# Kernel optimization log

Hardware: AMD Instinct MI355X
Metric: run time of the kernel (lower is better)

Reference implementation:

```python
import jax, jax.numpy as jnp
import numpy as np

N_NODES = 50000
N_EDGES = 1600000
N_PAIRS = 4096
IN_N, IN_E = 32, 8
H, OE, ON = 4, 8, 32  # heads, out_edge_feats, out_node_feats
L = 4  # layers


def setup_inputs() -> dict:
    key = jax.random.key(0)
    ks = jax.random.split(key, 20)
    s = 0.1
    return {
        "x": jax.random.normal(ks[0], (N_NODES, IN_N), jnp.float32),
        "e": jax.random.normal(ks[1], (N_EDGES, IN_E), jnp.float32),
        "W_ni": jax.random.normal(ks[2], (L, IN_N, H * OE), jnp.float32) * s,
        "W_nj": jax.random.normal(ks[3], (L, IN_N, H * OE), jnp.float32) * s,
        "W_fij": jax.random.normal(ks[4], (L, IN_E, H * OE), jnp.float32) * s,
        "b_edge": jax.random.normal(ks[5], (L, H * OE), jnp.float32) * s,
        "attn": jax.random.normal(ks[6], (L, H, OE), jnp.float32) * s,
        "W_node": jax.random.normal(ks[7], (L, IN_N, H * ON), jnp.float32) * s,
        "W1": jax.random.normal(ks[8], (2 * L * ON, 128), jnp.float32) * s,
        "b1": jax.random.normal(ks[9], (128,), jnp.float32) * s,
        "W2": jax.random.normal(ks[10], (128, 1), jnp.float32) * s,
        "b2": jax.random.normal(ks[11], (1,), jnp.float32) * s,
        "src": jax.random.randint(ks[12], (N_EDGES,), 0, N_NODES, jnp.int32),
        "dst": jax.random.randint(ks[13], (N_EDGES,), 0, N_NODES, jnp.int32),
        "users": jax.random.randint(ks[14], (N_PAIRS,), 0, N_NODES, jnp.int32),
        "items": jax.random.randint(ks[15], (N_PAIRS,), 0, N_NODES, jnp.int32),
    }


def _egat_layer(h, e, src, dst, W_ni, W_nj, W_fij, b_edge, attn, W_node, n_nodes):
    # per-edge edge features: f_ni[src] + f_nj[dst] + f_fij + bias  -> (E, H*OE)
    f = (h @ W_ni)[src] + (h @ W_nj)[dst] + e @ W_fij + b_edge
    f_out = jax.nn.leaky_relu(f).reshape(-1, H, OE)          # (E, H, OE)
    logits = jnp.einsum("ehd,hd->eh", f_out, attn)           # (E, H)
    # edge softmax over incoming edges of each dst node
    mx = jax.ops.segment_max(logits, dst, num_segments=n_nodes)
    z = jnp.exp(logits - mx[dst])
    denom = jax.ops.segment_sum(z, dst, num_segments=n_nodes)
    a = z / denom[dst]                                        # (E, H)
    hh = (h @ W_node).reshape(n_nodes, H, ON)                 # (N, H, ON)
    msg = hh[src] * a[:, :, None]                             # (E, H, ON)
    return jax.ops.segment_sum(msg, dst, num_segments=n_nodes)  # (N, H, ON)


def reference(x, e, W_ni, W_nj, W_fij, b_edge, attn, W_node, W1, b1, W2, b2,
              src, dst, users, items):
    n_nodes = x.shape[0]
    states = []
    h = x
    for l in range(L):
        agg = _egat_layer(h, e, src, dst, W_ni[l], W_nj[l], W_fij[l],
                          b_edge[l], attn[l], W_node[l], n_nodes)
        h = jax.nn.elu(agg.sum(axis=1))  # sum heads, ELU -> (N, ON)
        states.append(h)
    states = jnp.concatenate(states, axis=1)                  # (N, L*ON)
    z = jnp.concatenate([states[users], states[items]], axis=1)  # (B, 2*L*ON)
    z = jax.nn.relu(z @ W1 + b1)
    out = jax.nn.sigmoid(z @ W2 + b2)
    return out[:, 0]
```

## Files before the change

### kernel.cpp

```cpp
#include <hip/hip_runtime.h>
#include <math.h>


static __device__ inline unsigned short f2bf(float f) {
  unsigned x = __float_as_uint(f);
  unsigned r = x + 0x7fffu + ((x >> 16) & 1u);
  return (unsigned short)(r >> 16);
}
static __device__ inline unsigned pack2bf(float lo, float hi) {
  return (unsigned)f2bf(lo) | ((unsigned)f2bf(hi) << 16);
}
static __device__ inline float bf_lo(unsigned u) {
  return __uint_as_float(u << 16);
}
static __device__ inline float bf_hi(unsigned u) {
  return __uint_as_float(u & 0xffff0000u);
}


__global__ void zero_ints(int* __restrict__ p, int n) {
  int i = blockIdx.x * blockDim.x + threadIdx.x;
  if (i < n) p[i] = 0;
}

__global__ void histogram(const int* __restrict__ dst, int* __restrict__ hist,
                          int n_edges) {
  int e = blockIdx.x * blockDim.x + threadIdx.x;
  if (e < n_edges) atomicAdd(&hist[dst[e]], 1);
}

__global__ void scan_block(const int* __restrict__ hist, int* __restrict__ partial,
                           int* __restrict__ blocksum, int n) {
  __shared__ int buf[1024];
  int tid = threadIdx.x;
  int g = blockIdx.x * 1024 + tid;
  int v = (g < n) ? hist[g] : 0;
  buf[tid] = v;
  __syncthreads();
  for (int off = 1; off < 1024; off <<= 1) {
    int t = (tid >= off) ? buf[tid - off] : 0;
    __syncthreads();
    buf[tid] += t;
    __syncthreads();
  }
  if (g < n) partial[g] = buf[tid] - v;
  if (tid == 1023) blocksum[blockIdx.x] = buf[1023];
}

__global__ void scan_sums(int* __restrict__ blocksum, int nb) {
  if (threadIdx.x == 0 && blockIdx.x == 0) {
    int run = 0;
    for (int i = 0; i < nb; i++) {
      int t = blocksum[i];
      blocksum[i] = run;
      run += t;
    }
    blocksum[nb] = run;
  }
}

__global__ void scan_add(int* __restrict__ partial ,
                         const int* __restrict__ blocksum,
                         int* __restrict__ cursor, int n, int nb) {
  int g = blockIdx.x * blockDim.x + threadIdx.x;
  if (g < n) {
    int val = partial[g] + blocksum[g >> 10];
    partial[g] = val;
    cursor[g] = val;
  }
  if (g == 0) partial[n] = blocksum[nb];
}

#define FILL_NR 8
__global__ void fill_perm(const int* __restrict__ dst, int* __restrict__ cursor,
                          int* __restrict__ perm, int n_edges, int seg) {
  int range = blockIdx.x % FILL_NR;
  int group = blockIdx.x / FILL_NR;
  int ngroups = gridDim.x / FILL_NR;
  int lo = range * seg;
  int hi = lo + seg;
  int stride = ngroups * blockDim.x;
  for (int k = group * blockDim.x + threadIdx.x; k < n_edges; k += stride) {
    int d = dst[k];
    if (d >= lo && d < hi) {
      int p = atomicAdd(&cursor[d], 1);
      perm[p] = k;
    }
  }
}

__global__ void expand_sorted(const int* __restrict__ perm,
                              const int* __restrict__ src,
                              const int* __restrict__ dst,
                              const float* __restrict__ e,
                              int* __restrict__ src_s, int* __restrict__ dst_s,
                              uint4* __restrict__ e_s, int n_edges) {
  int k = blockIdx.x * blockDim.x + threadIdx.x;
  if (k >= n_edges) return;
  int eid = perm[k];
  src_s[k] = src[eid];
  dst_s[k] = dst[eid];
  const float4* ep = (const float4*)(e + (size_t)eid * 8);
  float4 a = ep[0], b = ep[1];
  uint4 r;
  r.x = pack2bf(a.x, a.y); r.y = pack2bf(a.z, a.w);
  r.z = pack2bf(b.x, b.y); r.w = pack2bf(b.z, b.w);
  e_s[k] = r;
}


__global__ void node_proj(const float* __restrict__ h,
                          const float* __restrict__ Wni,
                          const float* __restrict__ Wnj,
                          const float* __restrict__ Wnode,
                          const float* __restrict__ bE,
                          unsigned short* __restrict__ fni,
                          unsigned short* __restrict__ cdst,
                          unsigned short* __restrict__ hh, int n_nodes) {
  int wave = (blockIdx.x * blockDim.x + threadIdx.x) >> 6;
  int lane = threadIdx.x & 63;
  int nwaves = (gridDim.x * blockDim.x) >> 6;
  int j = lane & 31;
  const float* Wsel = (lane < 32) ? Wni : Wnj;
  for (int n = wave; n < n_nodes; n += nwaves) {
    const float* hrow = h + (size_t)n * 32;
    float a0 = 0.f, a1 = 0.f, a2 = 0.f;
#pragma unroll
    for (int k = 0; k < 32; k++) {
      float hv = hrow[k];
      a0 += hv * Wsel[k * 32 + j];
      a1 += hv * Wnode[k * 128 + lane];
      a2 += hv * Wnode[k * 128 + lane + 64];
    }
    if (lane < 32) fni[(size_t)n * 32 + j] = f2bf(a0);
    else           cdst[(size_t)n * 32 + j] = f2bf(a0 + bE[j]);
    hh[(size_t)n * 128 + lane] = f2bf(a1);
    hh[(size_t)n * 128 + lane + 64] = f2bf(a2);
  }
}

__global__ void edge_z(const int* __restrict__ src_s,
                       const int* __restrict__ dst_s,
                       const uint4* __restrict__ e_s,
                       const unsigned short* __restrict__ fni,
                       const unsigned short* __restrict__ cdst,
                       const float* __restrict__ Wf,
                       const float* __restrict__ attn,
                       float4* __restrict__ zrec, int n_edges) {
  __shared__ float wfl[256];
  __shared__ float atl[32];
  int tid = threadIdx.x;
  wfl[tid] = Wf[tid];
  if (tid < 32) atl[tid] = attn[tid];
  __syncthreads();
  int k = blockIdx.x * blockDim.x + tid;
  if (k >= n_edges) return;
  int s = src_s[k], d = dst_s[k];
  uint4 ep = e_s[k];
  float ev[8];
  ev[0] = bf_lo(ep.x); ev[1] = bf_hi(ep.x);
  ev[2] = bf_lo(ep.y); ev[3] = bf_hi(ep.y);
  ev[4] = bf_lo(ep.z); ev[5] = bf_hi(ep.z);
  ev[6] = bf_lo(ep.w); ev[7] = bf_hi(ep.w);
  const uint4* fr = (const uint4*)(fni + (size_t)s * 32);
  const uint4* cr = (const uint4*)(cdst + (size_t)d * 32);
  float f[32];
#pragma unroll
  for (int q = 0; q < 4; q++) {
    uint4 ua = fr[q], ub = cr[q];
    const unsigned* uap = (const unsigned*)&ua;
    const unsigned* ubp = (const unsigned*)&ub;
#pragma unroll
    for (int c = 0; c < 4; c++) {
      int jj = q * 8 + c * 2;
      f[jj]     = bf_lo(uap[c]) + bf_lo(ubp[c]);
      f[jj + 1] = bf_hi(uap[c]) + bf_hi(ubp[c]);
    }
  }
#pragma unroll
  for (int kk = 0; kk < 8; kk++) {
    float ek = ev[kk];
#pragma unroll
    for (int j4 = 0; j4 < 8; j4++) {
      float4 w = ((const float4*)wfl)[kk * 8 + j4];
      f[j4 * 4 + 0] = fmaf(ek, w.x, f[j4 * 4 + 0]);
      f[j4 * 4 + 1] = fmaf(ek, w.y, f[j4 * 4 + 1]);
      f[j4 * 4 + 2] = fmaf(ek, w.z, f[j4 * 4 + 2]);
      f[j4 * 4 + 3] = fmaf(ek, w.w, f[j4 * 4 + 3]);
    }
  }
  float lg[4] = {0.f, 0.f, 0.f, 0.f};
#pragma unroll
  for (int jj = 0; jj < 32; jj++) {
    float t = f[jj];
    t = (t >= 0.f) ? t : 0.01f * t;
    lg[jj >> 3] = fmaf(t, atl[jj], lg[jj >> 3]);
  }
  zrec[k] = make_float4(__expf(lg[0]), __expf(lg[1]),
                        __expf(lg[2]), __expf(lg[3]));
}

__global__ void node_agg(const float4* __restrict__ zrec,
                         const int* __restrict__ src_s,
                         const int* __restrict__ row_off,
                         const unsigned* __restrict__ hh,
                         float* __restrict__ hcur,
                         float* __restrict__ states,
                         int l, int n_nodes) {
  __shared__ float zw[4][64 * 4];
  __shared__ int sw[4][64];
  int wid = threadIdx.x >> 6;
  int lane = threadIdx.x & 63;
  int n = (blockIdx.x * blockDim.x + threadIdx.x) >> 6;
  if (n >= n_nodes) return;
  int base = row_off[n], end = row_off[n + 1];
  int head = lane >> 4;
  float* zwf = zw[wid];
  int* swp = sw[wid];
  float accx = 0.f, accy = 0.f;
  float sz0 = 0.f, sz1 = 0.f, sz2 = 0.f, sz3 = 0.f;

  for (int chunk = base; chunk < end; chunk += 64) {
    int k = chunk + lane;
    float4 zv4 = make_float4(0.f, 0.f, 0.f, 0.f);
    int sv = 0;
    if (k < end) { zv4 = zrec[k]; sv = src_s[k]; }
    ((float4*)zwf)[lane] = zv4;
    swp[lane] = sv;
    sz0 += zv4.x; sz1 += zv4.y; sz2 += zv4.z; sz3 += zv4.w;
    int cnt = min(64, end - chunk);

    int ee = 0;
    for (; ee + 8 <= cnt; ee += 8) {
      unsigned u[8];
      float zl[8];
#pragma unroll
      for (int i = 0; i < 8; i++) {
        int ss = __builtin_amdgcn_readfirstlane(swp[ee + i]);
        zl[i] = zwf[(ee + i) * 4 + head];
        u[i] = hh[(size_t)ss * 64 + lane];
      }
#pragma unroll
      for (int i = 0; i < 8; i++) {
        accx = fmaf(bf_lo(u[i]), zl[i], accx);
        accy = fmaf(bf_hi(u[i]), zl[i], accy);
      }
    }
    for (; ee < cnt; ee++) {
      int ss = __builtin_amdgcn_readfirstlane(swp[ee]);
      float zv = zwf[ee * 4 + head];
      unsigned u = hh[(size_t)ss * 64 + lane];
      accx = fmaf(bf_lo(u), zv, accx);
      accy = fmaf(bf_hi(u), zv, accy);
    }
  }

#pragma unroll
  for (int off = 32; off > 0; off >>= 1) {
    sz0 += __shfl_xor(sz0, off); sz1 += __shfl_xor(sz1, off);
    sz2 += __shfl_xor(sz2, off); sz3 += __shfl_xor(sz3, off);
  }
  float dh = (head == 0) ? sz0 : (head == 1) ? sz1 : (head == 2) ? sz2 : sz3;

  float vx = 0.f, vy = 0.f;
  if (dh > 0.f) { vx = accx / dh; vy = accy / dh; }
  vx += __shfl_xor(vx, 16); vx += __shfl_xor(vx, 32);
  vy += __shfl_xor(vy, 16); vy += __shfl_xor(vy, 32);
  if (lane < 16) {
    float rx = (vx > 0.f) ? vx : expm1f(vx);
    float ry = (vy > 0.f) ? vy : expm1f(vy);
    float2 r = make_float2(rx, ry);
    ((float2*)(hcur + (size_t)n * 32))[lane] = r;
    ((float2*)(states + (size_t)n * 128 + l * 32))[lane] = r;
  }
}

__global__ void mlp_head(const float* __restrict__ states,
                         const int* __restrict__ users, const int* __restrict__ items,
                         const float* __restrict__ W1, const float* __restrict__ b1,
                         const float* __restrict__ W2, const float* __restrict__ b2,
                         float* __restrict__ out, int n_pairs) {
  __shared__ float zin[256];
  __shared__ float red[2];
  int p = blockIdx.x;
  if (p >= n_pairs) return;
  int t = threadIdx.x;
  int u = users[p], it = items[p];
  zin[t] = states[(size_t)u * 128 + t];
  zin[t + 128] = states[(size_t)it * 128 + t];
  __syncthreads();
  float acc = b1[t];
#pragma unroll 8
  for (int i = 0; i < 256; i++) acc += zin[i] * W1[i * 128 + t];
  acc = acc > 0.f ? acc : 0.f;
  float c = acc * W2[t];
#pragma unroll
  for (int off = 32; off > 0; off >>= 1) c += __shfl_down(c, off);
  if ((t & 63) == 0) red[t >> 6] = c;
  __syncthreads();
  if (t == 0) {
    float sum = red[0] + red[1] + b2[0];
    out[p] = 1.f / (1.f + expf(-sum));
  }
}


extern "C" void kernel_launch(void* const* d_in, const int* in_sizes, int n_in,
                              void* d_out, int out_size, void* d_ws, size_t ws_size,
                              hipStream_t stream) {
  const float* x     = (const float*)d_in[0];
  const float* e     = (const float*)d_in[1];
  const float* W_ni  = (const float*)d_in[2];
  const float* W_nj  = (const float*)d_in[3];
  const float* W_fij = (const float*)d_in[4];
  const float* b_e   = (const float*)d_in[5];
  const float* attn  = (const float*)d_in[6];
  const float* W_nd  = (const float*)d_in[7];
  const float* W1    = (const float*)d_in[8];
  const float* b1    = (const float*)d_in[9];
  const float* W2    = (const float*)d_in[10];
  const float* b2    = (const float*)d_in[11];
  const int* src   = (const int*)d_in[12];
  const int* dst   = (const int*)d_in[13];
  const int* users = (const int*)d_in[14];
  const int* items = (const int*)d_in[15];
  float* out = (float*)d_out;

  int n_nodes = in_sizes[0] / 32;
  int n_edges = in_sizes[12];
  int n_pairs = in_sizes[14];

  char* wsb = (char*)d_ws;
  size_t off = 0;
  auto alloc = [&](size_t bytes) {
    char* p = wsb + off;
    off = (off + bytes + 255) & ~(size_t)255;
    return p;
  };
  float*          hcur   = (float*)alloc((size_t)n_nodes * 32 * 4);
  float*          states = (float*)alloc((size_t)n_nodes * 128 * 4);
  unsigned short* fni    = (unsigned short*)alloc((size_t)n_nodes * 32 * 2);
  unsigned short* cdst   = (unsigned short*)alloc((size_t)n_nodes * 32 * 2);
  unsigned short* hh     = (unsigned short*)alloc((size_t)n_nodes * 128 * 2);
  uint4*          e_s    = (uint4*)alloc((size_t)n_edges * 16);
  float4*         zrec   = (float4*)alloc((size_t)n_edges * 16);
  int*            src_s  = (int*)alloc((size_t)n_edges * 4);
  int*            dst_s  = (int*)alloc((size_t)n_edges * 4);
  int*            row_off  = (int*)alloc(((size_t)n_nodes + 8) * 4);
  int*            blocksum = (int*)alloc(256 * 4);
  int* perm   = (int*)zrec;
  int* hist   = (int*)((char*)zrec + ((size_t)n_edges * 4 + 1024));
  int* cursor = (int*)((char*)zrec + ((size_t)n_edges * 8 + 2048));

  int nb = (n_nodes + 1023) / 1024;
  int seg = (n_nodes + FILL_NR - 1) / FILL_NR;
  zero_ints<<<(n_nodes + 255) / 256, 256, 0, stream>>>(hist, n_nodes);
  histogram<<<(n_edges + 255) / 256, 256, 0, stream>>>(dst, hist, n_edges);
  scan_block<<<nb, 1024, 0, stream>>>(hist, row_off, blocksum, n_nodes);
  scan_sums<<<1, 64, 0, stream>>>(blocksum, nb);
  scan_add<<<(n_nodes + 255) / 256, 256, 0, stream>>>(row_off, blocksum, cursor,
                                                      n_nodes, nb);
  fill_perm<<<2048, 256, 0, stream>>>(dst, cursor, perm, n_edges, seg);
  expand_sorted<<<(n_edges + 255) / 256, 256, 0, stream>>>(
      perm, src, dst, e, src_s, dst_s, e_s, n_edges);

  for (int l = 0; l < 4; l++) {
    const float* hin = (l == 0) ? x : hcur;
    node_proj<<<2048, 256, 0, stream>>>(hin, W_ni + l * 1024, W_nj + l * 1024,
                                        W_nd + l * 4096, b_e + l * 32,
                                        fni, cdst, hh, n_nodes);
    edge_z<<<(n_edges + 255) / 256, 256, 0, stream>>>(
        src_s, dst_s, e_s, fni, cdst, W_fij + l * 256, attn + l * 32,
        zrec, n_edges);
    node_agg<<<(n_nodes * 64 + 255) / 256, 256, 0, stream>>>(
        zrec, src_s, row_off, (const unsigned*)hh, hcur, states, l, n_nodes);
  }
  mlp_head<<<n_pairs, 128, 0, stream>>>(states, users, items, W1, b1, W2, b2,
                                        out, n_pairs);
}
```

Baseline: 904.5 us.

## Split aggregation per head with head-planar layouts and XCD-aware block mapping

Stores hh and edge z values in head-major planes and replaces the single all-heads aggregation with a per-head kernel. Block indices are mapped so each XCD handles one head, which shrinks the gather working set per L2. A separate combine kernel sums the heads and applies ELU, states are stored as bf16, and the src/dst permutation is folded into fill_perm. The cost is an extra kernel launch per layer, an extra bf16 round trip for per-head partial results, and reduced precision.

```diff
diff --git a/kernel.cpp b/kernel.cpp
--- a/kernel.cpp
+++ b/kernel.cpp
@@ -9,6 +9,9 @@
 }
 static __device__ inline unsigned pack2bf(float lo, float hi) {
   return (unsigned)f2bf(lo) | ((unsigned)f2bf(hi) << 16);
+}
+static __device__ inline float bf2f(unsigned short u) {
+  return __uint_as_float(((unsigned)u) << 16);
 }
 static __device__ inline float bf_lo(unsigned u) {
   return __uint_as_float(u << 16);
@@ -72,8 +75,10 @@
 }
 
 #define FILL_NR 8
-__global__ void fill_perm(const int* __restrict__ dst, int* __restrict__ cursor,
-                          int* __restrict__ perm, int n_edges, int seg) {
+__global__ void fill_perm3(const int* __restrict__ dst, const int* __restrict__ src,
+                           int* __restrict__ cursor, int* __restrict__ perm,
+                           int* __restrict__ src_s, int* __restrict__ dst_s,
+                           int n_edges, int seg) {
   int range = blockIdx.x % FILL_NR;
   int group = blockIdx.x / FILL_NR;
   int ngroups = gridDim.x / FILL_NR;
@@ -85,21 +90,17 @@
     if (d >= lo && d < hi) {
       int p = atomicAdd(&cursor[d], 1);
       perm[p] = k;
-    }
-  }
-}
-
-__global__ void expand_sorted(const int* __restrict__ perm,
-                              const int* __restrict__ src,
-                              const int* __restrict__ dst,
-                              const float* __restrict__ e,
-                              int* __restrict__ src_s, int* __restrict__ dst_s,
-                              uint4* __restrict__ e_s, int n_edges) {
+      src_s[p] = src[k];
+      dst_s[p] = d;
+    }
+  }
+}
+
+__global__ void expand_e(const int* __restrict__ perm, const float* __restrict__ e,
+                         uint4* __restrict__ e_s, int n_edges) {
   int k = blockIdx.x * blockDim.x + threadIdx.x;
   if (k >= n_edges) return;
   int eid = perm[k];
-  src_s[k] = src[eid];
-  dst_s[k] = dst[eid];
   const float4* ep = (const float4*)(e + (size_t)eid * 8);
   float4 a = ep[0], b = ep[1];
   uint4 r;
@@ -116,11 +117,12 @@
                           const float* __restrict__ bE,
                           unsigned short* __restrict__ fni,
                           unsigned short* __restrict__ cdst,
-                          unsigned short* __restrict__ hh, int n_nodes) {
+                          unsigned short* __restrict__ hh_t, int n_nodes) {
   int wave = (blockIdx.x * blockDim.x + threadIdx.x) >> 6;
   int lane = threadIdx.x & 63;
   int nwaves = (gridDim.x * blockDim.x) >> 6;
   int j = lane & 31;
+  size_t plane = (size_t)n_nodes * 32;
   const float* Wsel = (lane < 32) ? Wni : Wnj;
   for (int n = wave; n < n_nodes; n += nwaves) {
     const float* hrow = h + (size_t)n * 32;
@@ -134,8 +136,10 @@
     }
     if (lane < 32) fni[(size_t)n * 32 + j] = f2bf(a0);
     else           cdst[(size_t)n * 32 + j] = f2bf(a0 + bE[j]);
-    hh[(size_t)n * 128 + lane] = f2bf(a1);
-    hh[(size_t)n * 128 + lane + 64] = f2bf(a2);
+    int h0 = lane >> 5;
+    int h1 = 2 + (lane >> 5);
+    hh_t[h0 * plane + (size_t)n * 32 + j] = f2bf(a1);
+    hh_t[h1 * plane + (size_t)n * 32 + j] = f2bf(a2);
   }
 }
 
@@ -146,7 +150,7 @@
                        const unsigned short* __restrict__ cdst,
                        const float* __restrict__ Wf,
                        const float* __restrict__ attn,
-                       float4* __restrict__ zrec, int n_edges) {
+                       float* __restrict__ zh, int n_edges) {
   __shared__ float wfl[256];
   __shared__ float atl[32];
   int tid = threadIdx.x;
@@ -196,86 +200,104 @@
     t = (t >= 0.f) ? t : 0.01f * t;
     lg[jj >> 3] = fmaf(t, atl[jj], lg[jj >> 3]);
   }
-  zrec[k] = make_float4(__expf(lg[0]), __expf(lg[1]),
-                        __expf(lg[2]), __expf(lg[3]));
-}
-
-__global__ void node_agg(const float4* __restrict__ zrec,
-                         const int* __restrict__ src_s,
-                         const int* __restrict__ row_off,
-                         const unsigned* __restrict__ hh,
-                         float* __restrict__ hcur,
-                         float* __restrict__ states,
-                         int l, int n_nodes) {
-  __shared__ float zw[4][64 * 4];
-  __shared__ int sw[4][64];
+  zh[k]                       = __expf(lg[0]);
+  zh[(size_t)n_edges + k]     = __expf(lg[1]);
+  zh[2 * (size_t)n_edges + k] = __expf(lg[2]);
+  zh[3 * (size_t)n_edges + k] = __expf(lg[3]);
+}
+
+__global__ void node_agg_head(const float* __restrict__ zh,
+                              const int* __restrict__ src_s,
+                              const int* __restrict__ row_off,
+                              const unsigned* __restrict__ hh_t,
+                              unsigned* __restrict__ outh,
+                              int n_nodes, int n_edges) {
+  __shared__ float zb[4][64];
+  __shared__ int sb[4][64];
   int wid = threadIdx.x >> 6;
   int lane = threadIdx.x & 63;
-  int n = (blockIdx.x * blockDim.x + threadIdx.x) >> 6;
+  int xcd = blockIdx.x & 7;
+  int head = xcd >> 1;
+  int i = (blockIdx.x >> 3) * 2 + (xcd & 1);
+  int n = i * 4 + wid;
   if (n >= n_nodes) return;
+  const float* z = zh + (size_t)head * n_edges;
+  const unsigned* hs = hh_t + (size_t)head * n_nodes * 16;
+  float* zw = zb[wid];
+  int* sw = sb[wid];
+  int g = lane >> 4, fl = lane & 15;
   int base = row_off[n], end = row_off[n + 1];
-  int head = lane >> 4;
-  float* zwf = zw[wid];
-  int* swp = sw[wid];
-  float accx = 0.f, accy = 0.f;
-  float sz0 = 0.f, sz1 = 0.f, sz2 = 0.f, sz3 = 0.f;
+  float accx = 0.f, accy = 0.f, sz = 0.f;
 
   for (int chunk = base; chunk < end; chunk += 64) {
     int k = chunk + lane;
-    float4 zv4 = make_float4(0.f, 0.f, 0.f, 0.f);
+    float zv = 0.f;
     int sv = 0;
-    if (k < end) { zv4 = zrec[k]; sv = src_s[k]; }
-    ((float4*)zwf)[lane] = zv4;
-    swp[lane] = sv;
-    sz0 += zv4.x; sz1 += zv4.y; sz2 += zv4.z; sz3 += zv4.w;
+    if (k < end) { zv = z[k]; sv = src_s[k]; }
+    zw[lane] = zv;
+    sw[lane] = sv;
+    sz += zv;
     int cnt = min(64, end - chunk);
-
+    int iters = (cnt + 3) >> 2;
     int ee = 0;
-    for (; ee + 8 <= cnt; ee += 8) {
-      unsigned u[8];
-      float zl[8];
-#pragma unroll
-      for (int i = 0; i < 8; i++) {
-        int ss = __builtin_amdgcn_readfirstlane(swp[ee + i]);
-        zl[i] = zwf[(ee + i) * 4 + head];
-        u[i] = hh[(size_t)ss * 64 + lane];
+    for (; ee + 4 <= iters; ee += 4) {
+      unsigned u[4];
+      float zl[4];
+#pragma unroll
+      for (int t = 0; t < 4; t++) {
+        int idx = (ee + t) * 4 + g;
+        zl[t] = zw[idx];
+        int ss = sw[idx];
+        u[t] = hs[(size_t)ss * 16 + fl];
       }
 #pragma unroll
-      for (int i = 0; i < 8; i++) {
-        accx = fmaf(bf_lo(u[i]), zl[i], accx);
-        accy = fmaf(bf_hi(u[i]), zl[i], accy);
+      for (int t = 0; t < 4; t++) {
+        accx = fmaf(bf_lo(u[t]), zl[t], accx);
+        accy = fmaf(bf_hi(u[t]), zl[t], accy);
       }
     }
-    for (; ee < cnt; ee++) {
-      int ss = __builtin_amdgcn_readfirstlane(swp[ee]);
-      float zv = zwf[ee * 4 + head];
-      unsigned u = hh[(size_t)ss * 64 + lane];
-      accx = fmaf(bf_lo(u), zv, accx);
-      accy = fmaf(bf_hi(u), zv, accy);
-    }
-  }
-
-#pragma unroll
-  for (int off = 32; off > 0; off >>= 1) {
-    sz0 += __shfl_xor(sz0, off); sz1 += __shfl_xor(sz1, off);
-    sz2 += __shfl_xor(sz2, off); sz3 += __shfl_xor(sz3, off);
-  }
-  float dh = (head == 0) ? sz0 : (head == 1) ? sz1 : (head == 2) ? sz2 : sz3;
-
-  float vx = 0.f, vy = 0.f;
-  if (dh > 0.f) { vx = accx / dh; vy = accy / dh; }
-  vx += __shfl_xor(vx, 16); vx += __shfl_xor(vx, 32);
-  vy += __shfl_xor(vy, 16); vy += __shfl_xor(vy, 32);
+    for (; ee < iters; ee++) {
+      int idx = ee * 4 + g;
+      float zl = zw[idx];
+      int ss = sw[idx];
+      unsigned u = hs[(size_t)ss * 16 + fl];
+      accx = fmaf(bf_lo(u), zl, accx);
+      accy = fmaf(bf_hi(u), zl, accy);
+    }
+  }
+
+#pragma unroll
+  for (int off = 32; off > 0; off >>= 1) sz += __shfl_xor(sz, off);
+  accx += __shfl_xor(accx, 16); accx += __shfl_xor(accx, 32);
+  accy += __shfl_xor(accy, 16); accy += __shfl_xor(accy, 32);
   if (lane < 16) {
-    float rx = (vx > 0.f) ? vx : expm1f(vx);
-    float ry = (vy > 0.f) ? vy : expm1f(vy);
-    float2 r = make_float2(rx, ry);
-    ((float2*)(hcur + (size_t)n * 32))[lane] = r;
-    ((float2*)(states + (size_t)n * 128 + l * 32))[lane] = r;
-  }
-}
-
-__global__ void mlp_head(const float* __restrict__ states,
+    float ax = 0.f, ay = 0.f;
+    if (sz > 0.f) { ax = accx / sz; ay = accy / sz; }
+    outh[((size_t)head * n_nodes + n) * 16 + fl] = pack2bf(ax, ay);
+  }
+}
+
+__global__ void combine(const unsigned* __restrict__ outh,
+                        float* __restrict__ hcur,
+                        unsigned* __restrict__ states_u,
+                        int l, int n_nodes) {
+  int idx = blockIdx.x * blockDim.x + threadIdx.x;
+  if (idx >= n_nodes * 16) return;
+  int n = idx >> 4, fl = idx & 15;
+  size_t plane = (size_t)n_nodes * 16;
+  unsigned a0 = outh[(size_t)n * 16 + fl];
+  unsigned a1 = outh[plane + (size_t)n * 16 + fl];
+  unsigned a2 = outh[2 * plane + (size_t)n * 16 + fl];
+  unsigned a3 = outh[3 * plane + (size_t)n * 16 + fl];
+  float vx = bf_lo(a0) + bf_lo(a1) + bf_lo(a2) + bf_lo(a3);
+  float vy = bf_hi(a0) + bf_hi(a1) + bf_hi(a2) + bf_hi(a3);
+  float rx = (vx > 0.f) ? vx : expm1f(vx);
+  float ry = (vy > 0.f) ? vy : expm1f(vy);
+  ((float2*)(hcur + (size_t)n * 32))[fl] = make_float2(rx, ry);
+  states_u[(size_t)n * 64 + l * 16 + fl] = pack2bf(rx, ry);
+}
+
+__global__ void mlp_head(const unsigned short* __restrict__ states,
                          const int* __restrict__ users, const int* __restrict__ items,
                          const float* __restrict__ W1, const float* __restrict__ b1,
                          const float* __restrict__ W2, const float* __restrict__ b2,
@@ -286,8 +308,8 @@
   if (p >= n_pairs) return;
   int t = threadIdx.x;
   int u = users[p], it = items[p];
-  zin[t] = states[(size_t)u * 128 + t];
-  zin[t + 128] = states[(size_t)it * 128 + t];
+  zin[t] = bf2f(states[(size_t)u * 128 + t]);
+  zin[t + 128] = bf2f(states[(size_t)it * 128 + t]);
   __syncthreads();
   float acc = b1[t];
 #pragma unroll 8
@@ -338,19 +360,20 @@
     return p;
   };
   float*          hcur   = (float*)alloc((size_t)n_nodes * 32 * 4);
-  float*          states = (float*)alloc((size_t)n_nodes * 128 * 4);
+  unsigned*       states = (unsigned*)alloc((size_t)n_nodes * 64 * 4);
   unsigned short* fni    = (unsigned short*)alloc((size_t)n_nodes * 32 * 2);
   unsigned short* cdst   = (unsigned short*)alloc((size_t)n_nodes * 32 * 2);
-  unsigned short* hh     = (unsigned short*)alloc((size_t)n_nodes * 128 * 2);
+  unsigned short* hh_t   = (unsigned short*)alloc((size_t)n_nodes * 128 * 2);
   uint4*          e_s    = (uint4*)alloc((size_t)n_edges * 16);
-  float4*         zrec   = (float4*)alloc((size_t)n_edges * 16);
+  float*          zh     = (float*)alloc((size_t)n_edges * 4 * 4);
+  unsigned*       outh   = (unsigned*)alloc((size_t)n_nodes * 64 * 4);
   int*            src_s  = (int*)alloc((size_t)n_edges * 4);
   int*            dst_s  = (int*)alloc((size_t)n_edges * 4);
   int*            row_off  = (int*)alloc(((size_t)n_nodes + 8) * 4);
   int*            blocksum = (int*)alloc(256 * 4);
-  int* perm   = (int*)zrec;
-  int* hist   = (int*)((char*)zrec + ((size_t)n_edges * 4 + 1024));
-  int* cursor = (int*)((char*)zrec + ((size_t)n_edges * 8 + 2048));
+  int* perm   = (int*)outh;
+  int* hist   = (int*)((char*)outh + ((size_t)n_edges * 4 + 1024));
+  int* cursor = (int*)((char*)outh + ((size_t)n_edges * 4 + (size_t)(n_nodes + 16) * 4 + 2048));
 
   int nb = (n_nodes + 1023) / 1024;
   int seg = (n_nodes + FILL_NR - 1) / FILL_NR;
@@ -360,21 +383,24 @@
   scan_sums<<<1, 64, 0, stream>>>(blocksum, nb);
   scan_add<<<(n_nodes + 255) / 256, 256, 0, stream>>>(row_off, blocksum, cursor,
                                                       n_nodes, nb);
-  fill_perm<<<2048, 256, 0, stream>>>(dst, cursor, perm, n_edges, seg);
-  expand_sorted<<<(n_edges + 255) / 256, 256, 0, stream>>>(
-      perm, src, dst, e, src_s, dst_s, e_s, n_edges);
-
+  fill_perm3<<<2048, 256, 0, stream>>>(dst, src, cursor, perm, src_s, dst_s,
+                                       n_edges, seg);
+  expand_e<<<(n_edges + 255) / 256, 256, 0, stream>>>(perm, e, e_s, n_edges);
+
+  int aggblocks = 8 * ((((n_nodes + 3) / 4) + 1) / 2);
   for (int l = 0; l < 4; l++) {
     const float* hin = (l == 0) ? x : hcur;
     node_proj<<<2048, 256, 0, stream>>>(hin, W_ni + l * 1024, W_nj + l * 1024,
                                         W_nd + l * 4096, b_e + l * 32,
-                                        fni, cdst, hh, n_nodes);
+                                        fni, cdst, hh_t, n_nodes);
     edge_z<<<(n_edges + 255) / 256, 256, 0, stream>>>(
         src_s, dst_s, e_s, fni, cdst, W_fij + l * 256, attn + l * 32,
-        zrec, n_edges);
-    node_agg<<<(n_nodes * 64 + 255) / 256, 256, 0, stream>>>(
-        zrec, src_s, row_off, (const unsigned*)hh, hcur, states, l, n_nodes);
-  }
-  mlp_head<<<n_pairs, 128, 0, stream>>>(states, users, items, W1, b1, W2, b2,
-                                        out, n_pairs);
-}
+        zh, n_edges);
+    node_agg_head<<<aggblocks, 256, 0, stream>>>(
+        zh, src_s, row_off, (const unsigned*)hh_t, outh, n_nodes, n_edges);
+    combine<<<(n_nodes * 16 + 255) / 256, 256, 0, stream>>>(
+        outh, hcur, states, l, n_nodes);
+  }
+  mlp_head<<<n_pairs, 128, 0, stream>>>((const unsigned short*)states, users,
+                                        items, W1, b1, W2, b2, out, n_pairs);
+}
```

Measured after the change: 985.8 us. 1.09x slower.
